# Optimization experiments

Hardware: AMD Instinct MI355X
Metric: run time of the kernel (lower is better)

The kernel has to match this reference:

```python
import jax, jax.numpy as jnp
import numpy as np

D_IN = 1024
D_OUT = 1024
NUM_HEADS = 16
HEAD_DIM = D_OUT // NUM_HEADS


def setup_inputs() -> dict:
    key = jax.random.key(0)
    kx, kq, kk, kv, ko = jax.random.split(key, 5)
    s = 1.0 / np.sqrt(D_IN)
    return {
        "x": jax.random.normal(kx, (1, 4096, D_IN), dtype=jnp.float32),
        "Wq": jax.random.normal(kq, (D_IN, D_OUT), dtype=jnp.float32) * s,
        "Wk": jax.random.normal(kk, (D_IN, D_OUT), dtype=jnp.float32) * s,
        "Wv": jax.random.normal(kv, (D_IN, D_OUT), dtype=jnp.float32) * s,
        "Wo": jax.random.normal(ko, (D_OUT, D_OUT), dtype=jnp.float32) * s,
    }


def reference(x, Wq, Wk, Wv, Wo):
    b, s, _ = x.shape
    # project and split heads: [b, h, s, d]
    def split_heads(t):
        return t.reshape(b, s, NUM_HEADS, HEAD_DIM).transpose(0, 2, 1, 3)
    Q = split_heads(x @ Wq)
    K = split_heads(x @ Wk)
    V = split_heads(x @ Wv)
    scores = jnp.einsum("bhqd,bhkd->bhqk", Q, K) / jnp.sqrt(jnp.float32(HEAD_DIM))
    causal = jnp.triu(jnp.ones((s, s), dtype=bool), k=1)  # True above diagonal
    scores = jnp.where(causal, -jnp.inf, scores)
    probs = jax.nn.softmax(scores, axis=-1)
    out = jnp.einsum("bhqk,bhkd->bhqd", probs, V)
    out = out.transpose(0, 2, 1, 3).reshape(b, s, D_OUT)
    return out @ Wo
```

## Files before the change

### kernel.cpp

```cpp
#include <hip/hip_runtime.h>
#include <cstdint>

#define S_LEN 4096
#define D_MODEL 1024
#define NHEAD 16
#define HDIM 64

typedef __bf16 bf16_t;
typedef __bf16 bf16x8 __attribute__((ext_vector_type(8)));
typedef __bf16 bf16x4 __attribute__((ext_vector_type(4)));
typedef float floatx4 __attribute__((ext_vector_type(4)));

#define QSCALE 0.18033688011112042f

__device__ __forceinline__ void lds_cp16(void* lds, const void* g) {
    __builtin_amdgcn_global_load_lds(
        (const __attribute__((address_space(1))) unsigned int*)g,
        (__attribute__((address_space(3))) unsigned int*)lds,
        16, 0, 0);
}

__global__ __launch_bounds__(256) void k_prep(const float* __restrict__ x,
                                              const float* __restrict__ Wq,
                                              const float* __restrict__ Wk,
                                              const float* __restrict__ Wv,
                                              const float* __restrict__ Wo,
                                              bf16_t* __restrict__ xb,
                                              bf16_t* __restrict__ WtQKV,
                                              bf16_t* __restrict__ WtO) {
    const int bx = blockIdx.x;
    if (bx < 4096) {
        int i = bx * 256 + threadIdx.x;
        float4 v = ((const float4*)x)[i];
        bf16x4 o;
        o[0] = (bf16_t)v.x; o[1] = (bf16_t)v.y; o[2] = (bf16_t)v.z; o[3] = (bf16_t)v.w;
        *(bf16x4*)(xb + (size_t)i * 4) = o;
        return;
    }
    __shared__ float lds[64][65];
    const int i = bx - 4096;
    const int z = i >> 8, rem = i & 255;
    const float* W = (z == 0) ? Wq : (z == 1) ? Wk : (z == 2) ? Wv : Wo;
    bf16_t* Wt = (z < 3) ? (WtQKV + (size_t)z * 1048576) : WtO;
    const int k0 = (rem >> 4) * 64, n0 = (rem & 15) * 64;
    const int t = threadIdx.x, cl = t & 63, rl = t >> 6;
#pragma unroll
    for (int r = 0; r < 16; ++r)
        lds[r * 4 + rl][cl] = W[(size_t)(k0 + r * 4 + rl) * 1024 + n0 + cl];
    __syncthreads();
#pragma unroll
    for (int r = 0; r < 16; ++r)
        Wt[(size_t)(n0 + r * 4 + rl) * 1024 + k0 + cl] = (bf16_t)lds[cl][r * 4 + rl];
}

template <int MODE>
__global__ __launch_bounds__(256) void k_gemm(const bf16_t* __restrict__ A,
                                              const bf16_t* __restrict__ Bt,
                                              float* __restrict__ Cout,
                                              bf16_t* __restrict__ Qb,
                                              bf16_t* __restrict__ Kb,
                                              bf16_t* __restrict__ Vt) {
    __shared__ __align__(16) bf16_t sA[128 * 32];
    __shared__ __align__(16) bf16_t sB[128 * 32];
    const int t = threadIdx.x, w = t >> 6, lane = t & 63, quad = lane >> 4, l15 = lane & 15;
    const int m0 = blockIdx.x * 128, n0 = blockIdx.y * 128;
    const int wm = w >> 1, wn = w & 1;

    floatx4 acc[4][4];
#pragma unroll
    for (int i = 0; i < 4; ++i)
#pragma unroll
        for (int j = 0; j < 4; ++j)
            acc[i][j] = floatx4{0.f, 0.f, 0.f, 0.f};

    for (int kb = 0; kb < 32; ++kb) {
        __syncthreads();
#pragma unroll
        for (int r = 0; r < 2; ++r) {
            int c = t + 256 * r;
            int row = c >> 2, kq = c & 3;
            lds_cp16(&sA[w * 512 + r * 2048],
                     A + (size_t)(m0 + row) * 1024 + kb * 32 + kq * 8);
            lds_cp16(&sB[w * 512 + r * 2048],
                     Bt + (size_t)(n0 + row) * 1024 + kb * 32 + kq * 8);
        }
        __syncthreads();
        bf16x8 af[4], bfr[4];
#pragma unroll
        for (int i = 0; i < 4; ++i)
            af[i] = *(const bf16x8*)&sA[(wm * 64 + i * 16 + l15) * 32 + quad * 8];
#pragma unroll
        for (int j = 0; j < 4; ++j)
            bfr[j] = *(const bf16x8*)&sB[(wn * 64 + j * 16 + l15) * 32 + quad * 8];
#pragma unroll
        for (int i = 0; i < 4; ++i)
#pragma unroll
            for (int j = 0; j < 4; ++j)
                acc[i][j] = __builtin_amdgcn_mfma_f32_16x16x32_bf16(af[i], bfr[j],
                                                                    acc[i][j], 0, 0, 0);
    }

    const int mrow = m0 + wm * 64 + quad * 4;
    if (MODE == 0) {
        const int ncol = n0 + wn * 64 + l15;
#pragma unroll
        for (int i = 0; i < 4; ++i)
#pragma unroll
            for (int j = 0; j < 4; ++j)
#pragma unroll
                for (int r = 0; r < 4; ++r)
                    Cout[(size_t)(mrow + i * 16 + r) * 1024 + ncol + j * 16] = acc[i][j][r];
    } else {
        const int g = (int)blockIdx.y >> 3;
        const int ncbase = ((int)blockIdx.y & 7) * 128 + wn * 64 + l15;
        if (g == 2) {
#pragma unroll
            for (int j = 0; j < 4; ++j) {
                int nc = ncbase + j * 16;
                int hh = nc >> 6, dd = nc & 63;
                bf16_t* dst = Vt + (size_t)hh * 262144 + (size_t)dd * 64;
#pragma unroll
                for (int i = 0; i < 4; ++i) {
                    int s0r = mrow + i * 16;
                    bf16x4 pk;
                    pk[0] = (bf16_t)acc[i][j][0]; pk[1] = (bf16_t)acc[i][j][1];
                    pk[2] = (bf16_t)acc[i][j][2]; pk[3] = (bf16_t)acc[i][j][3];
                    int kk = s0r & 63;
                    int pp = (kk & 0x20) | ((kk & 0xC) << 1) | ((kk & 0x10) >> 2);
                    *(bf16x4*)&dst[(size_t)(s0r >> 6) * 4096 + pp] = pk;
                }
            }
        } else {
            bf16_t* base = g ? Kb : Qb;
            const float sc = g ? 1.0f : QSCALE;
#pragma unroll
            for (int j = 0; j < 4; ++j) {
                int nc = ncbase + j * 16;
                int hh = nc >> 6, dd = nc & 63;
#pragma unroll
                for (int i = 0; i < 4; ++i)
#pragma unroll
                    for (int r = 0; r < 4; ++r)
                        base[(size_t)hh * 262144 + (size_t)(mrow + i * 16 + r) * 64 + dd] =
                            (bf16_t)(acc[i][j][r] * sc);
            }
        }
    }
}

__global__ __launch_bounds__(256, 4) void k_attn(const bf16_t* __restrict__ Qb,
                                                 const bf16_t* __restrict__ Kb,
                                                 const bf16_t* __restrict__ Vt,
                                                 bf16_t* __restrict__ OP0,
                                                 bf16_t* __restrict__ OP1,
                                                 float* __restrict__ Lp) {
    __shared__ __align__(16) bf16_t Ks[2][64 * 64];
    __shared__ __align__(16) bf16_t Vts[64 * 64];
    const int bid = blockIdx.x;
    const int slot = bid >> 8, jj = bid & 255, g = jj >> 5, u = jj & 31;
    const int h = u >> 1, sp = u & 1;
    const int qb = (slot == 0) ? (31 - g) : (slot == 1) ? (16 + g)
                 : (slot == 2) ? (15 - g) : g;
    const int t = threadIdx.x, w = t >> 6, quad = (t & 63) >> 4, l15 = t & 15;
    const bf16_t* Qh = Qb + (size_t)h * 262144;
    const bf16_t* Kh = Kb + (size_t)h * 262144;
    const bf16_t* Vth = Vt + (size_t)h * 262144;

    const bf16_t* Qrow = Qh + (size_t)(qb * 128 + w * 32 + l15) * 64;
    bf16x8 bq[2][2];
#pragma unroll
    for (int qt = 0; qt < 2; ++qt)
#pragma unroll
        for (int kh = 0; kh < 2; ++kh)
            bq[qt][kh] = *(const bf16x8*)(Qrow + qt * 1024 + kh * 32 + quad * 8);

    float l_s[2] = {0.f, 0.f};
    floatx4 o_acc[2][4];
#pragma unroll
    for (int qt = 0; qt < 2; ++qt)
#pragma unroll
        for (int j = 0; j < 4; ++j) o_acc[qt][j] = floatx4{0.f, 0.f, 0.f, 0.f};

#define STAGE_K(b, kb_)                                                            \
    {                                                                              \
        _Pragma("unroll") for (int r = 0; r < 2; ++r) {                            \
            int c = t + 256 * r;                                                   \
            int row = c >> 3, sw = (c & 7) ^ (row & 7);                            \
            lds_cp16(&Ks[b][c * 8], Kh + (size_t)(kb_) * 4096 + row * 64 + sw * 8);\
        }                                                                          \
    }
#define STAGE_V(kb_)                                                               \
    {                                                                              \
        _Pragma("unroll") for (int r = 0; r < 2; ++r) {                            \
            int c = t + 256 * r;                                                   \
            int row = c >> 3, sw = (c & 7) ^ (row & 7);                            \
            lds_cp16(&Vts[c * 8], Vth + (size_t)(kb_) * 4096 + row * 64 + sw * 8); \
        }                                                                          \
    }

    const int t0 = sp ? (qb + 1) : 0;
    const int nIter = qb + 1;
    const int qmax = qb * 128 + w * 32 + 31;

    STAGE_K(0, t0)
    for (int it = 0; it < nIter; ++it) {
        const int kb = t0 + it;
        const int buf = it & 1;
        __syncthreads();
        STAGE_V(kb)
        if (it + 1 < nIter) STAGE_K(buf ^ 1, kb + 1)
        const bool active = (kb * 64 <= qmax);

        bf16x8 pa[2][2];
        if (active) {
            floatx4 st[2][4];
#pragma unroll
            for (int j = 0; j < 4; ++j) {
                int rk = j * 16 + l15;
                bf16x8 a0 = *(const bf16x8*)&Ks[buf][rk * 64 + ((quad ^ (rk & 7)) * 8)];
                bf16x8 a1 = *(const bf16x8*)&Ks[buf][rk * 64 + (((quad + 4) ^ (rk & 7)) * 8)];
#pragma unroll
                for (int qt = 0; qt < 2; ++qt) {
                    floatx4 z = {0.f, 0.f, 0.f, 0.f};
                    st[qt][j] = __builtin_amdgcn_mfma_f32_16x16x32_bf16(a0, bq[qt][0], z, 0, 0, 0);
                    st[qt][j] = __builtin_amdgcn_mfma_f32_16x16x32_bf16(a1, bq[qt][1], st[qt][j], 0, 0, 0);
                }
            }
            if (kb >= 2 * qb) {
#pragma unroll
                for (int qt = 0; qt < 2; ++qt) {
                    int qg = qb * 128 + w * 32 + qt * 16 + l15;
#pragma unroll
                    for (int j = 0; j < 4; ++j)
#pragma unroll
                        for (int r = 0; r < 4; ++r) {
                            int keyg = kb * 64 + j * 16 + quad * 4 + r;
                            if (keyg > qg) st[qt][j][r] = -1e30f;
                        }
                }
            }
#pragma unroll
            for (int qt = 0; qt < 2; ++qt) {
                float a0 = 0.f, a1 = 0.f, a2 = 0.f, a3 = 0.f;
#pragma unroll
                for (int j = 0; j < 4; ++j) {
                    st[qt][j][0] = exp2f(st[qt][j][0]); a0 += st[qt][j][0];
                    st[qt][j][1] = exp2f(st[qt][j][1]); a1 += st[qt][j][1];
                    st[qt][j][2] = exp2f(st[qt][j][2]); a2 += st[qt][j][2];
                    st[qt][j][3] = exp2f(st[qt][j][3]); a3 += st[qt][j][3];
                }
                l_s[qt] += (a0 + a1) + (a2 + a3);
#pragma unroll
                for (int kh = 0; kh < 2; ++kh)
#pragma unroll
                    for (int m = 0; m < 4; ++m) {
                        pa[qt][kh][m]     = (bf16_t)st[qt][2 * kh][m];
                        pa[qt][kh][4 + m] = (bf16_t)st[qt][2 * kh + 1][m];
                    }
            }
        }
        if (it + 1 < nIter) asm volatile("s_waitcnt vmcnt(2)" ::: "memory");
        else                asm volatile("s_waitcnt vmcnt(0)" ::: "memory");
        if (active) {
#pragma unroll
            for (int kh = 0; kh < 2; ++kh) {
                int pc = kh * 4 + quad;
#pragma unroll
                for (int j = 0; j < 4; ++j) {
                    int rd = j * 16 + l15;
                    bf16x8 bv = *(const bf16x8*)&Vts[rd * 64 + ((pc ^ (rd & 7)) * 8)];
                    o_acc[0][j] = __builtin_amdgcn_mfma_f32_16x16x32_bf16(pa[0][kh], bv, o_acc[0][j], 0, 0, 0);
                    o_acc[1][j] = __builtin_amdgcn_mfma_f32_16x16x32_bf16(pa[1][kh], bv, o_acc[1][j], 0, 0, 0);
                }
            }
        }
    }
    bf16_t* OPx = sp ? OP1 : OP0;
#pragma unroll
    for (int qt = 0; qt < 2; ++qt) {
        float l = l_s[qt];
        l += __shfl_xor(l, 16);
        l += __shfl_xor(l, 32);
        if (quad == 0)
            Lp[sp * 65536 + h * 4096 + (qb * 128 + w * 32 + qt * 16 + l15)] = l;
#pragma unroll
        for (int r = 0; r < 4; ++r) {
            int rowg = qb * 128 + w * 32 + qt * 16 + quad * 4 + r;
#pragma unroll
            for (int j = 0; j < 4; ++j)
                OPx[(size_t)rowg * 1024 + h * 64 + j * 16 + l15] = (bf16_t)o_acc[qt][j][r];
        }
    }
#undef STAGE_K
#undef STAGE_V
}

__global__ __launch_bounds__(256) void k_combine(const bf16_t* __restrict__ OP0,
                                                 const bf16_t* __restrict__ OP1,
                                                 const float* __restrict__ Lp,
                                                 bf16_t* __restrict__ Ob) {
    int gi = (blockIdx.x * 256 + threadIdx.x) * 4;
    int q = gi >> 10, hh = (gi & 1023) >> 6;
    float inv = 1.0f / (Lp[hh * 4096 + q] + Lp[65536 + hh * 4096 + q]);
    bf16x4 a = *(const bf16x4*)(OP0 + gi);
    bf16x4 b = *(const bf16x4*)(OP1 + gi);
    bf16x4 o;
#pragma unroll
    for (int r = 0; r < 4; ++r)
        o[r] = (bf16_t)(((float)a[r] + (float)b[r]) * inv);
    *(bf16x4*)(Ob + gi) = o;
}

extern "C" void kernel_launch(void* const* d_in, const int* in_sizes, int n_in,
                              void* d_out, int out_size, void* d_ws, size_t ws_size,
                              hipStream_t stream) {
    const float* x  = (const float*)d_in[0];
    const float* Wq = (const float*)d_in[1];
    const float* Wk = (const float*)d_in[2];
    const float* Wv = (const float*)d_in[3];
    const float* Wo = (const float*)d_in[4];

    bf16_t* ws = (bf16_t*)d_ws;
    bf16_t* Xb    = ws;
    bf16_t* WtQKV = Xb + 4194304;
    bf16_t* WtO   = WtQKV + 3145728;
    bf16_t* Qb    = WtO + 1048576;
    bf16_t* Kb    = Qb + 4194304;
    bf16_t* Vt    = Kb + 4194304;
    bf16_t* Ob    = Vt + 4194304;
    bf16_t* OP1   = Ob + 4194304;
    bf16_t* OP0   = Xb;
    float*  Lp    = (float*)WtQKV;
    float* out = (float*)d_out;

    k_prep<<<5120, 256, 0, stream>>>(x, Wq, Wk, Wv, Wo, Xb, WtQKV, WtO);
    k_gemm<1><<<dim3(32, 24), 256, 0, stream>>>(Xb, WtQKV, nullptr, Qb, Kb, Vt);
    k_attn<<<1024, 256, 0, stream>>>(Qb, Kb, Vt, OP0, OP1, Lp);
    k_combine<<<4096, 256, 0, stream>>>(OP0, OP1, Lp, Ob);
    k_gemm<0><<<dim3(32, 8), 256, 0, stream>>>(Ob, WtO, out, nullptr, nullptr, nullptr);
}
```

Baseline: 203.2 us.

## Double-buffer V in attention, add setprio and fast exp, shrink output GEMM tile

The attention kernel now double-buffers the V tile alongside K and prefetches both for the next iteration. This removes the mid-iteration vmcnt wait on V. It also wraps the MFMA sections in s_setprio and replaces exp2f with a raw v_exp_f32. The output projection GEMM is templated to a 64-row M tile, doubling its grid to 512 blocks for better CU fill. The trade-offs are extra LDS per attention block (which may reduce occupancy), the loss of exp2f's denormal handling, and less data reuse per block in the smaller GEMM tile.

```diff
diff --git a/kernel.cpp b/kernel.cpp
--- a/kernel.cpp
+++ b/kernel.cpp
@@ -18,6 +18,12 @@
         (const __attribute__((address_space(1))) unsigned int*)g,
         (__attribute__((address_space(3))) unsigned int*)lds,
         16, 0, 0);
+}
+
+__device__ __forceinline__ float fast_exp2(float x) {
+    float r;
+    asm("v_exp_f32 %0, %1" : "=v"(r) : "v"(x));
+    return r;
 }
 
 __global__ __launch_bounds__(256) void k_prep(const float* __restrict__ x,
@@ -53,22 +59,23 @@
         Wt[(size_t)(n0 + r * 4 + rl) * 1024 + k0 + cl] = (bf16_t)lds[cl][r * 4 + rl];
 }
 
-template <int MODE>
+template <int MODE, int MT>
 __global__ __launch_bounds__(256) void k_gemm(const bf16_t* __restrict__ A,
                                               const bf16_t* __restrict__ Bt,
                                               float* __restrict__ Cout,
                                               bf16_t* __restrict__ Qb,
                                               bf16_t* __restrict__ Kb,
                                               bf16_t* __restrict__ Vt) {
-    __shared__ __align__(16) bf16_t sA[128 * 32];
+    constexpr int MI = MT / 32;
+    __shared__ __align__(16) bf16_t sA[MT * 32];
     __shared__ __align__(16) bf16_t sB[128 * 32];
     const int t = threadIdx.x, w = t >> 6, lane = t & 63, quad = lane >> 4, l15 = lane & 15;
-    const int m0 = blockIdx.x * 128, n0 = blockIdx.y * 128;
+    const int m0 = blockIdx.x * MT, n0 = blockIdx.y * 128;
     const int wm = w >> 1, wn = w & 1;
 
-    floatx4 acc[4][4];
-#pragma unroll
-    for (int i = 0; i < 4; ++i)
+    floatx4 acc[MI][4];
+#pragma unroll
+    for (int i = 0; i < MI; ++i)
 #pragma unroll
         for (int j = 0; j < 4; ++j)
             acc[i][j] = floatx4{0.f, 0.f, 0.f, 0.f};
@@ -76,35 +83,40 @@
     for (int kb = 0; kb < 32; ++kb) {
         __syncthreads();
 #pragma unroll
-        for (int r = 0; r < 2; ++r) {
+        for (int r = 0; r < MT / 64; ++r) {
             int c = t + 256 * r;
             int row = c >> 2, kq = c & 3;
             lds_cp16(&sA[w * 512 + r * 2048],
                      A + (size_t)(m0 + row) * 1024 + kb * 32 + kq * 8);
+        }
+#pragma unroll
+        for (int r = 0; r < 2; ++r) {
+            int c = t + 256 * r;
+            int row = c >> 2, kq = c & 3;
             lds_cp16(&sB[w * 512 + r * 2048],
                      Bt + (size_t)(n0 + row) * 1024 + kb * 32 + kq * 8);
         }
         __syncthreads();
-        bf16x8 af[4], bfr[4];
-#pragma unroll
-        for (int i = 0; i < 4; ++i)
-            af[i] = *(const bf16x8*)&sA[(wm * 64 + i * 16 + l15) * 32 + quad * 8];
+        bf16x8 af[MI], bfr[4];
+#pragma unroll
+        for (int i = 0; i < MI; ++i)
+            af[i] = *(const bf16x8*)&sA[(wm * (MT / 2) + i * 16 + l15) * 32 + quad * 8];
 #pragma unroll
         for (int j = 0; j < 4; ++j)
             bfr[j] = *(const bf16x8*)&sB[(wn * 64 + j * 16 + l15) * 32 + quad * 8];
 #pragma unroll
-        for (int i = 0; i < 4; ++i)
+        for (int i = 0; i < MI; ++i)
 #pragma unroll
             for (int j = 0; j < 4; ++j)
                 acc[i][j] = __builtin_amdgcn_mfma_f32_16x16x32_bf16(af[i], bfr[j],
                                                                     acc[i][j], 0, 0, 0);
     }
 
-    const int mrow = m0 + wm * 64 + quad * 4;
+    const int mrow = m0 + wm * (MT / 2) + quad * 4;
     if (MODE == 0) {
         const int ncol = n0 + wn * 64 + l15;
 #pragma unroll
-        for (int i = 0; i < 4; ++i)
+        for (int i = 0; i < MI; ++i)
 #pragma unroll
             for (int j = 0; j < 4; ++j)
 #pragma unroll
@@ -120,7 +132,7 @@
                 int hh = nc >> 6, dd = nc & 63;
                 bf16_t* dst = Vt + (size_t)hh * 262144 + (size_t)dd * 64;
 #pragma unroll
-                for (int i = 0; i < 4; ++i) {
+                for (int i = 0; i < MI; ++i) {
                     int s0r = mrow + i * 16;
                     bf16x4 pk;
                     pk[0] = (bf16_t)acc[i][j][0]; pk[1] = (bf16_t)acc[i][j][1];
@@ -138,7 +150,7 @@
                 int nc = ncbase + j * 16;
                 int hh = nc >> 6, dd = nc & 63;
 #pragma unroll
-                for (int i = 0; i < 4; ++i)
+                for (int i = 0; i < MI; ++i)
 #pragma unroll
                     for (int r = 0; r < 4; ++r)
                         base[(size_t)hh * 262144 + (size_t)(mrow + i * 16 + r) * 64 + dd] =
@@ -155,7 +167,7 @@
                                                  bf16_t* __restrict__ OP1,
                                                  float* __restrict__ Lp) {
     __shared__ __align__(16) bf16_t Ks[2][64 * 64];
-    __shared__ __align__(16) bf16_t Vts[64 * 64];
+    __shared__ __align__(16) bf16_t Vts[2][64 * 64];
     const int bid = blockIdx.x;
     const int slot = bid >> 8, jj = bid & 255, g = jj >> 5, u = jj & 31;
     const int h = u >> 1, sp = u & 1;
@@ -189,12 +201,12 @@
             lds_cp16(&Ks[b][c * 8], Kh + (size_t)(kb_) * 4096 + row * 64 + sw * 8);\
         }                                                                          \
     }
-#define STAGE_V(kb_)                                                               \
+#define STAGE_V(b, kb_)                                                            \
     {                                                                              \
         _Pragma("unroll") for (int r = 0; r < 2; ++r) {                            \
             int c = t + 256 * r;                                                   \
             int row = c >> 3, sw = (c & 7) ^ (row & 7);                            \
-            lds_cp16(&Vts[c * 8], Vth + (size_t)(kb_) * 4096 + row * 64 + sw * 8); \
+            lds_cp16(&Vts[b][c * 8], Vth + (size_t)(kb_) * 4096 + row * 64 + sw * 8);\
         }                                                                          \
     }
 
@@ -203,17 +215,20 @@
     const int qmax = qb * 128 + w * 32 + 31;
 
     STAGE_K(0, t0)
+    STAGE_V(0, t0)
     for (int it = 0; it < nIter; ++it) {
         const int kb = t0 + it;
         const int buf = it & 1;
         __syncthreads();
-        STAGE_V(kb)
-        if (it + 1 < nIter) STAGE_K(buf ^ 1, kb + 1)
+        if (it + 1 < nIter) {
+            STAGE_K(buf ^ 1, kb + 1)
+            STAGE_V(buf ^ 1, kb + 1)
+        }
         const bool active = (kb * 64 <= qmax);
 
-        bf16x8 pa[2][2];
         if (active) {
             floatx4 st[2][4];
+            __builtin_amdgcn_s_setprio(1);
 #pragma unroll
             for (int j = 0; j < 4; ++j) {
                 int rk = j * 16 + l15;
@@ -226,6 +241,7 @@
                     st[qt][j] = __builtin_amdgcn_mfma_f32_16x16x32_bf16(a1, bq[qt][1], st[qt][j], 0, 0, 0);
                 }
             }
+            __builtin_amdgcn_s_setprio(0);
             if (kb >= 2 * qb) {
 #pragma unroll
                 for (int qt = 0; qt < 2; ++qt) {
@@ -239,15 +255,16 @@
                         }
                 }
             }
+            bf16x8 pa[2][2];
 #pragma unroll
             for (int qt = 0; qt < 2; ++qt) {
                 float a0 = 0.f, a1 = 0.f, a2 = 0.f, a3 = 0.f;
 #pragma unroll
                 for (int j = 0; j < 4; ++j) {
-                    st[qt][j][0] = exp2f(st[qt][j][0]); a0 += st[qt][j][0];
-                    st[qt][j][1] = exp2f(st[qt][j][1]); a1 += st[qt][j][1];
-                    st[qt][j][2] = exp2f(st[qt][j][2]); a2 += st[qt][j][2];
-                    st[qt][j][3] = exp2f(st[qt][j][3]); a3 += st[qt][j][3];
+                    st[qt][j][0] = fast_exp2(st[qt][j][0]); a0 += st[qt][j][0];
+                    st[qt][j][1] = fast_exp2(st[qt][j][1]); a1 += st[qt][j][1];
+                    st[qt][j][2] = fast_exp2(st[qt][j][2]); a2 += st[qt][j][2];
+                    st[qt][j][3] = fast_exp2(st[qt][j][3]); a3 += st[qt][j][3];
                 }
                 l_s[qt] += (a0 + a1) + (a2 + a3);
 #pragma unroll
@@ -258,21 +275,19 @@
                         pa[qt][kh][4 + m] = (bf16_t)st[qt][2 * kh + 1][m];
                     }
             }
-        }
-        if (it + 1 < nIter) asm volatile("s_waitcnt vmcnt(2)" ::: "memory");
-        else                asm volatile("s_waitcnt vmcnt(0)" ::: "memory");
-        if (active) {
+            __builtin_amdgcn_s_setprio(1);
 #pragma unroll
             for (int kh = 0; kh < 2; ++kh) {
                 int pc = kh * 4 + quad;
 #pragma unroll
                 for (int j = 0; j < 4; ++j) {
                     int rd = j * 16 + l15;
-                    bf16x8 bv = *(const bf16x8*)&Vts[rd * 64 + ((pc ^ (rd & 7)) * 8)];
+                    bf16x8 bv = *(const bf16x8*)&Vts[buf][rd * 64 + ((pc ^ (rd & 7)) * 8)];
                     o_acc[0][j] = __builtin_amdgcn_mfma_f32_16x16x32_bf16(pa[0][kh], bv, o_acc[0][j], 0, 0, 0);
                     o_acc[1][j] = __builtin_amdgcn_mfma_f32_16x16x32_bf16(pa[1][kh], bv, o_acc[1][j], 0, 0, 0);
                 }
             }
+            __builtin_amdgcn_s_setprio(0);
         }
     }
     bf16_t* OPx = sp ? OP1 : OP0;
@@ -334,8 +349,8 @@
     float* out = (float*)d_out;
 
     k_prep<<<5120, 256, 0, stream>>>(x, Wq, Wk, Wv, Wo, Xb, WtQKV, WtO);
-    k_gemm<1><<<dim3(32, 24), 256, 0, stream>>>(Xb, WtQKV, nullptr, Qb, Kb, Vt);
+    k_gemm<1, 128><<<dim3(32, 24), 256, 0, stream>>>(Xb, WtQKV, nullptr, Qb, Kb, Vt);
     k_attn<<<1024, 256, 0, stream>>>(Qb, Kb, Vt, OP0, OP1, Lp);
     k_combine<<<4096, 256, 0, stream>>>(OP0, OP1, Lp, Ob);
-    k_gemm<0><<<dim3(32, 8), 256, 0, stream>>>(Ob, WtO, out, nullptr, nullptr, nullptr);
-}
+    k_gemm<0, 64><<<dim3(64, 8), 256, 0, stream>>>(Ob, WtO, out, nullptr, nullptr, nullptr);
+}
```

Result: faster. 188.4 us (-7.3%).
